# Performance work log

Hardware: AMD Instinct MI355X
Metric: run time of the kernel (lower is better)

The kernel has to match this reference:

```python
import jax, jax.numpy as jnp
import numpy as np

N = 100000
LS = (0, 1, 2)
MULS = (128, 64, 32)   # multiplicities of 0e,1o,2e in input1 / mid / out
MUL_Y = 64             # input2 = 64x0e (pure scalars)
DIM_X = sum(m * (2 * l + 1) for m, l in zip(MULS, LS))  # 480


def _split_irreps(x):
    # x: (N, 480) -> list of (N, mul, 2l+1) blocks
    parts, off = [], 0
    for m, l in zip(MULS, LS):
        d = m * (2 * l + 1)
        parts.append(x[:, off:off + d].reshape(-1, m, 2 * l + 1))
        off += d
    return parts


def setup_inputs() -> dict:
    key = jax.random.key(0)
    ks = jax.random.split(key, 8)
    inp = {
        "x": jax.random.normal(ks[0], (N, DIM_X), jnp.float32),
        "y": jax.random.normal(ks[1], (N, MUL_Y), jnp.float32),
    }
    for i, m in enumerate(MULS):
        # e3nn internal weights ~ N(0,1); path normalization applied in forward
        inp[f"W_tp{i}"] = jax.random.normal(ks[2 + i], (m, MUL_Y, m), jnp.float32)
        inp[f"W_lin{i}"] = jax.random.normal(ks[5 + i], (m, m), jnp.float32)
    return inp


def reference(x, y, W_tp0, W_tp1, W_tp2, W_lin0, W_lin1, W_lin2):
    W_tp = (W_tp0, W_tp1, W_tp2)
    W_lin = (W_lin0, W_lin1, W_lin2)
    xs = _split_irreps(x)
    outs = []
    for m, l, Wt, Wl, xl in zip(MULS, LS, W_tp, W_lin, xs):
        # e3nn 'uvw' path with scalar (0e) second input:
        #   CG(l,0,l)[m1,0,mo] = delta / sqrt(2l+1)
        #   path_weight = sqrt(ir_out.dim / (mul1*mul2)) = sqrt((2l+1)/(m*MUL_Y))
        # net coefficient = 1 / sqrt(m * MUL_Y)
        c_tp = float(1.0 / np.sqrt(m * MUL_Y))
        mid = c_tp * jnp.einsum('uvw,num,nv->nwm', Wt, xl, y)  # (N, m, 2l+1)
        # o3.Linear: single path per irrep, weight 1/sqrt(fan_in), fan_in = m
        c_lin = float(1.0 / np.sqrt(m))
        out = c_lin * jnp.einsum('uw,num->nwm', Wl, mid)       # (N, m, 2l+1)
        outs.append(out.reshape(-1, m * (2 * l + 1)))
    return jnp.concatenate(outs, axis=-1)  # (N, 480)
```

## Files before the change

kernel.cpp:

```cpp
#include <hip/hip_runtime.h>


typedef _Float16 f16x8 __attribute__((ext_vector_type(8)));
typedef _Float16 h2    __attribute__((ext_vector_type(2)));
typedef float    f32x4 __attribute__((ext_vector_type(4)));

template<int M, int NT>
__global__ void pack_b(const float* __restrict__ Wt, const float* __restrict__ Wl,
                       _Float16* __restrict__ Bp) {
    const int gid = blockIdx.x * 256 + threadIdx.x;
    const int total = M * 64 * M / 2;
    if (gid >= total) return;
    const int w_ = gid & (M - 1);
    const int uvp = gid / M;
    const float4* wtA = (const float4*)(Wt + (size_t)(2 * uvp) * M);
    const float4* wtB = (const float4*)(Wt + (size_t)(2 * uvp + 1) * M);
    float a0 = 0.f, a1 = 0.f;
    #pragma unroll 4
    for (int w = 0; w < M; w += 4) {
        float4 tA = wtA[w >> 2], tB = wtB[w >> 2];
        float l0 = Wl[(w + 0) * M + w_], l1 = Wl[(w + 1) * M + w_];
        float l2 = Wl[(w + 2) * M + w_], l3 = Wl[(w + 3) * M + w_];
        a0 += tA.x * l0 + tA.y * l1 + tA.z * l2 + tA.w * l3;
        a1 += tB.x * l0 + tB.y * l1 + tB.z * l2 + tB.w * l3;
    }
    #pragma unroll
    for (int t = 0; t < 2; ++t) {
        const int uv = 2 * uvp + t;
        const int u = uv >> 6, v = uv & 63;
        const int vh = v >> 5, vv = v & 31, quad = vv >> 3, j = vv & 7;
        const int kc = vh * M + u, nt = w_ >> 4, lane = quad * 16 + (w_ & 15);
        Bp[((size_t)(kc * NT + nt) * 64 + lane) * 8 + j] = (_Float16)(t ? a1 : a0);
    }
}

template<int M, int NCOMP, int XOFF, int NT, int MT, int WAVES_N, int LOGM>
__device__ __forceinline__ void tp_block(char* smem, int wg,
    const float* __restrict__ x, const float* __restrict__ y,
    const _Float16* __restrict__ Bp, float* __restrict__ out, int Rtot, float cscale)
{
    constexpr int YS = 80;
    constexpr int YROWS = (MT + NCOMP - 2) / NCOMP + 1;
    constexpr int KTOT = 2 * M;
    constexpr int SWZ = (2 * M >= 128) ? 8 : (2 * M) / 16;
    constexpr int WAVES_M = 4 / WAVES_N;
    constexpr int WM = (MT / 16) / WAVES_M;
    constexpr int WN = NT / WAVES_N;

    char* xb = smem;
    _Float16* yl = (_Float16*)(smem + MT * M * 2);
    const int tid = threadIdx.x;
    const int r0 = wg * MT;
    const int s0 = r0 / NCOMP;

    for (int idx = tid; idx < M * MT; idx += 256) {
        const int u = idx & (M - 1);
        const int row = idx >> LOGM;
        const int R = r0 + row;
        float v = 0.f;
        if (R < Rtot) {
            const int s = (unsigned)R / NCOMP;
            const int k = R - s * NCOMP;
            v = x[(size_t)s * 480 + XOFF + u * NCOMP + k];
        }
        const int off = ((row * M + u) * 2) ^ ((row & (SWZ - 1)) << 4);
        *(_Float16*)(xb + off) = (_Float16)v;
    }
    for (int idx = tid; idx < YROWS * 64; idx += 256) {
        const int v_ = idx & 63;
        const int row = idx >> 6;
        const int s = s0 + row;
        float val = 0.f;
        if (s * NCOMP < Rtot) val = y[(size_t)s * 64 + v_];
        yl[row * YS + v_] = (_Float16)val;
    }
    __syncthreads();

    const int lane = tid & 63;
    const int wv = tid >> 6;
    const int wni = wv % WAVES_N;
    const int wmi = wv / WAVES_N;
    const int l15 = lane & 15;
    const int quad = lane >> 4;

    int rowf[WM], xoffb[WM], yoffs[WM];
    #pragma unroll
    for (int f = 0; f < WM; ++f) {
        rowf[f] = (wmi * WM + f) * 16 + l15;
        xoffb[f] = (rowf[f] * M * 2) ^ ((rowf[f] & (SWZ - 1)) << 4);
        const int sloc = (int)((unsigned)(r0 + rowf[f]) / NCOMP) - s0;
        yoffs[f] = sloc * YS + quad * 8;
    }

    f32x4 acc[WM][WN];
    #pragma unroll
    for (int f = 0; f < WM; ++f)
        #pragma unroll
        for (int g = 0; g < WN; ++g) acc[f][g] = f32x4{0.f, 0.f, 0.f, 0.f};

    const char* bpc = (const char*)Bp;
    constexpr unsigned BSTRIDE = (unsigned)NT * 64 * 16;
    const unsigned lane_b = ((unsigned)(wni * WN) * 64 + lane) * 16;
    const unsigned bmax = (unsigned)(KTOT - 1) * BSTRIDE + lane_b;

    f16x8 bpp[2][WN];
    #pragma unroll
    for (int g = 0; g < WN; ++g) {
        bpp[0][g] = *(const f16x8*)(bpc + lane_b + g * 1024);
        bpp[1][g] = *(const f16x8*)(bpc + BSTRIDE + lane_b + g * 1024);
    }
    unsigned boff = 2 * BSTRIDE + lane_b;

    f16x8 xf[WM];
    uint4  yh[WM];

    #pragma unroll 1
    for (int g8 = 0; g8 < KTOT; g8 += 8) {
        const int u0 = g8 & (M - 1);
        #pragma unroll
        for (int f = 0; f < WM; ++f)
            xf[f] = *(const f16x8*)(xb + (xoffb[f] ^ (u0 * 2)));
        if (u0 == 0) {
            const int vh = g8 >> LOGM;
            #pragma unroll
            for (int f = 0; f < WM; ++f)
                yh[f] = *(const uint4*)(yl + yoffs[f] + vh * 32);
        }
        #pragma unroll
        for (int j = 0; j < 8; ++j) {
            f16x8 af[WM];
            #pragma unroll
            for (int f = 0; f < WM; ++f) {
                const _Float16 xh = xf[f][j];
                h2 xbb; xbb[0] = xh; xbb[1] = xh;
                union { uint4 u4; h2 h[4]; } yv; yv.u4 = yh[f];
                union { f16x8 v8; h2 h[4]; } a_;
                #pragma unroll
                for (int q = 0; q < 4; ++q) a_.h[q] = xbb * yv.h[q];
                af[f] = a_.v8;
            }
            #pragma unroll
            for (int f = 0; f < WM; ++f)
                #pragma unroll
                for (int g = 0; g < WN; ++g)
                    acc[f][g] = __builtin_amdgcn_mfma_f32_16x16x32_f16(af[f], bpp[j & 1][g], acc[f][g], 0, 0, 0);
            {
                const unsigned bo = boff < bmax ? boff : bmax;
                #pragma unroll
                for (int g = 0; g < WN; ++g)
                    bpp[j & 1][g] = *(const f16x8*)(bpc + bo + g * 1024);
                boff += BSTRIDE;
            }
        }
    }

    #pragma unroll
    for (int f = 0; f < WM; ++f) {
        #pragma unroll
        for (int g = 0; g < WN; ++g) {
            const int col = (wni * WN + g) * 16 + l15;
            #pragma unroll
            for (int r = 0; r < 4; ++r) {
                const int R = r0 + (wmi * WM + f) * 16 + quad * 4 + r;
                if (R < Rtot) {
                    const int s = (unsigned)R / NCOMP;
                    const int k = R - s * NCOMP;
                    out[(size_t)s * 480 + XOFF + col * NCOMP + k] = acc[f][g][r] * cscale;
                }
            }
        }
    }
}

__global__ __launch_bounds__(256, 3)
void tp_main(const float* __restrict__ x, const float* __restrict__ y,
             const _Float16* __restrict__ B0, const _Float16* __restrict__ B1,
             const _Float16* __restrict__ B2, float* __restrict__ out,
             int R0, int R1, int R2, int G0, int G1)
{
    __shared__ char smem[53248];
    const int b = blockIdx.x;
    if (b < G0)            tp_block<128, 1,   0, 8, 128, 2, 7>(smem, b,           x, y, B0, out, R0, 1.f / 1024.f);
    else if (b < G0 + G1)  tp_block< 64, 3, 128, 4, 128, 2, 6>(smem, b - G0,      x, y, B1, out, R1, 1.f / 512.f);
    else                   tp_block< 32, 5, 320, 2, 256, 1, 5>(smem, b - G0 - G1, x, y, B2, out, R2, 1.f / 256.f);
}

extern "C" void kernel_launch(void* const* d_in, const int* in_sizes, int n_in,
                              void* d_out, int out_size, void* d_ws, size_t ws_size,
                              hipStream_t stream) {
    const float* x   = (const float*)d_in[0];
    const float* y   = (const float*)d_in[1];
    const float* Wt0 = (const float*)d_in[2];
    const float* Wl0 = (const float*)d_in[3];
    const float* Wt1 = (const float*)d_in[4];
    const float* Wl1 = (const float*)d_in[5];
    const float* Wt2 = (const float*)d_in[6];
    const float* Wl2 = (const float*)d_in[7];
    float* out = (float*)d_out;

    const int Ns = in_sizes[0] / 480;

    _Float16* B0 = (_Float16*)d_ws;
    _Float16* B1 = B0 + 8192 * 128;
    _Float16* B2 = B1 + 4096 * 64;

    pack_b<128, 8><<<(128 * 64 * 128 / 2 + 255) / 256, 256, 0, stream>>>(Wt0, Wl0, B0);
    pack_b< 64, 4><<<( 64 * 64 *  64 / 2 + 255) / 256, 256, 0, stream>>>(Wt1, Wl1, B1);
    pack_b< 32, 2><<<( 32 * 64 *  32 / 2 + 255) / 256, 256, 0, stream>>>(Wt2, Wl2, B2);

    const int R0 = Ns, R1 = Ns * 3, R2 = Ns * 5;
    const int G0 = (R0 + 127) / 128;
    const int G1 = (R1 + 127) / 128;
    const int G2 = (R2 + 255) / 256;
    tp_main<<<G0 + G1 + G2, 256, 0, stream>>>(x, y, B0, B1, B2, out, R0, R1, R2, G0, G1);
}
```

Before: 818.5 us.

## Stage B tiles in LDS with async double buffering and larger row tiles

Reorders the packed B layout so K is interleaved by (u, v-half). The main loop now streams B chunks into LDS through global_load_lds with double buffering, instead of every wave loading B from global memory into registers. x is staged in 16-column slabs through a register prefetch and double-buffered LDS, and y is held directly in registers. Blocks grow to 512 threads and 384 or 512 rows, and each wave covers all N columns, so each B load is reused across more rows. The cost is one __syncthreads per K chunk, more registers per wave, and a larger LDS footprint per block, which limits how many blocks fit on a CU.

```diff
diff --git a/kernel.cpp b/kernel.cpp
--- a/kernel.cpp
+++ b/kernel.cpp
@@ -4,6 +4,12 @@
 typedef _Float16 f16x8 __attribute__((ext_vector_type(8)));
 typedef _Float16 h2    __attribute__((ext_vector_type(2)));
 typedef float    f32x4 __attribute__((ext_vector_type(4)));
+
+__device__ __forceinline__ void gload_lds16(const void* g, void* l) {
+    __builtin_amdgcn_global_load_lds(
+        (const __attribute__((address_space(1))) unsigned*)g,
+        (__attribute__((address_space(3))) unsigned*)l, 16, 0, 0);
+}
 
 template<int M, int NT>
 __global__ void pack_b(const float* __restrict__ Wt, const float* __restrict__ Wl,
@@ -29,141 +35,176 @@
         const int uv = 2 * uvp + t;
         const int u = uv >> 6, v = uv & 63;
         const int vh = v >> 5, vv = v & 31, quad = vv >> 3, j = vv & 7;
-        const int kc = vh * M + u, nt = w_ >> 4, lane = quad * 16 + (w_ & 15);
+        const int kc = u * 2 + vh, nt = w_ >> 4, lane = quad * 16 + (w_ & 15);
         Bp[((size_t)(kc * NT + nt) * 64 + lane) * 8 + j] = (_Float16)(t ? a1 : a0);
     }
 }
 
-template<int M, int NCOMP, int XOFF, int NT, int MT, int WAVES_N, int LOGM>
+template<int M, int NCOMP, int XOFF, int NT, int KC, int MT>
 __device__ __forceinline__ void tp_block(char* smem, int wg,
     const float* __restrict__ x, const float* __restrict__ y,
     const _Float16* __restrict__ Bp, float* __restrict__ out, int Rtot, float cscale)
 {
-    constexpr int YS = 80;
-    constexpr int YROWS = (MT + NCOMP - 2) / NCOMP + 1;
+    constexpr int WM = MT / 128;
+    constexpr int WN = NT;
+    constexpr int UC = KC / 2;
+    constexpr int XU = 16;
     constexpr int KTOT = 2 * M;
-    constexpr int SWZ = (2 * M >= 128) ? 8 : (2 * M) / 16;
-    constexpr int WAVES_M = 4 / WAVES_N;
-    constexpr int WM = (MT / 16) / WAVES_M;
-    constexpr int WN = NT / WAVES_N;
-
-    char* xb = smem;
-    _Float16* yl = (_Float16*)(smem + MT * M * 2);
+    constexpr int NCHUNK = KTOT / KC;
+    constexpr int CPS = XU / UC;
+    constexpr int NSLAB = M / XU;
+    constexpr int BCH = KC * NT * 1024;
+    constexpr int XSL = MT * XU * 2;
+    constexpr int NS_T = MT / NCOMP + 2;
+    constexpr int XE = NS_T * XU * NCOMP;
+    constexpr int XITER = (XE + 511) / 512;
+
+    char* bb0 = smem;
+    char* bb1 = smem + BCH;
+    char* xb0 = smem + 2 * BCH;
+    char* xb1 = smem + 2 * BCH + XSL;
+
     const int tid = threadIdx.x;
+    const int lane = tid & 63;
+    const int wv = tid >> 6;
+    const int l15 = lane & 15;
+    const int quad = lane >> 4;
     const int r0 = wg * MT;
     const int s0 = r0 / NCOMP;
-
-    for (int idx = tid; idx < M * MT; idx += 256) {
-        const int u = idx & (M - 1);
-        const int row = idx >> LOGM;
-        const int R = r0 + row;
-        float v = 0.f;
-        if (R < Rtot) {
-            const int s = (unsigned)R / NCOMP;
-            const int k = R - s * NCOMP;
-            v = x[(size_t)s * 480 + XOFF + u * NCOMP + k];
-        }
-        const int off = ((row * M + u) * 2) ^ ((row & (SWZ - 1)) << 4);
-        *(_Float16*)(xb + off) = (_Float16)v;
-    }
-    for (int idx = tid; idx < YROWS * 64; idx += 256) {
-        const int v_ = idx & 63;
-        const int row = idx >> 6;
-        const int s = s0 + row;
-        float val = 0.f;
-        if (s * NCOMP < Rtot) val = y[(size_t)s * 64 + v_];
-        yl[row * YS + v_] = (_Float16)val;
-    }
+    const int k0 = r0 - s0 * NCOMP;
+
+    float xt[XITER];
+    auto xld = [&](int slab) {
+        const int ub = slab * XU;
+        #pragma unroll
+        for (int i = 0; i < XITER; ++i) {
+            const int p = tid + i * 512;
+            float v = 0.f;
+            if (p < XE) {
+                const int sl = p / (XU * NCOMP);
+                const int fo = p - sl * (XU * NCOMP);
+                const int ul = fo / NCOMP;
+                const int k  = fo - ul * NCOMP;
+                const int rl = sl * NCOMP + k - k0;
+                if (rl >= 0 && rl < MT && (r0 + rl) < Rtot)
+                    v = x[(size_t)(s0 + sl) * 480 + XOFF + (ub + ul) * NCOMP + k];
+            }
+            xt[i] = v;
+        }
+    };
+    auto xwr = [&](char* xd) {
+        #pragma unroll
+        for (int i = 0; i < XITER; ++i) {
+            const int p = tid + i * 512;
+            if (p < XE) {
+                const int sl = p / (XU * NCOMP);
+                const int fo = p - sl * (XU * NCOMP);
+                const int ul = fo / NCOMP;
+                const int k  = fo - ul * NCOMP;
+                const int rl = sl * NCOMP + k - k0;
+                if (rl >= 0 && rl < MT)
+                    *(_Float16*)(xd + (rl * XU + ul) * 2) = (_Float16)xt[i];
+            }
+        }
+    };
+    auto stageB = [&](int c, char* bd) {
+        const char* gs = (const char*)Bp + (size_t)c * BCH + wv * 2048 + lane * 16;
+        char* ld = bd + wv * 2048;
+        gload_lds16(gs, ld);
+        gload_lds16(gs + 1024, ld + 1024);
+    };
+
+    int rowf[WM];
+    union YH { f16x8 v; h2 h[4]; };
+    YH yh[2][WM];
+    #pragma unroll
+    for (int f = 0; f < WM; ++f) {
+        rowf[f] = wv * (WM * 16) + f * 16 + l15;
+        const int Rg = r0 + rowf[f];
+        const int sf = (Rg < Rtot) ? (int)((unsigned)Rg / NCOMP) : 0;
+        #pragma unroll
+        for (int vh = 0; vh < 2; ++vh) {
+            const float4* yp = (const float4*)(y + (size_t)sf * 64 + vh * 32 + quad * 8);
+            const float4 a = yp[0], b = yp[1];
+            union { f16x8 v; _Float16 e[8]; } t;
+            t.e[0] = (_Float16)a.x; t.e[1] = (_Float16)a.y;
+            t.e[2] = (_Float16)a.z; t.e[3] = (_Float16)a.w;
+            t.e[4] = (_Float16)b.x; t.e[5] = (_Float16)b.y;
+            t.e[6] = (_Float16)b.z; t.e[7] = (_Float16)b.w;
+            yh[vh][f].v = t.v;
+        }
+    }
+
+    f32x4 acc[WM][WN];
+    #pragma unroll
+    for (int f = 0; f < WM; ++f)
+        #pragma unroll
+        for (int g = 0; g < WN; ++g) acc[f][g] = f32x4{0.f, 0.f, 0.f, 0.f};
+
+    xld(0);
+    stageB(0, bb0);
+    xwr(xb0);
     __syncthreads();
 
-    const int lane = tid & 63;
-    const int wv = tid >> 6;
-    const int wni = wv % WAVES_N;
-    const int wmi = wv / WAVES_N;
-    const int l15 = lane & 15;
-    const int quad = lane >> 4;
-
-    int rowf[WM], xoffb[WM], yoffs[WM];
-    #pragma unroll
-    for (int f = 0; f < WM; ++f) {
-        rowf[f] = (wmi * WM + f) * 16 + l15;
-        xoffb[f] = (rowf[f] * M * 2) ^ ((rowf[f] & (SWZ - 1)) << 4);
-        const int sloc = (int)((unsigned)(r0 + rowf[f]) / NCOMP) - s0;
-        yoffs[f] = sloc * YS + quad * 8;
-    }
-
-    f32x4 acc[WM][WN];
-    #pragma unroll
-    for (int f = 0; f < WM; ++f)
-        #pragma unroll
-        for (int g = 0; g < WN; ++g) acc[f][g] = f32x4{0.f, 0.f, 0.f, 0.f};
-
-    const char* bpc = (const char*)Bp;
-    constexpr unsigned BSTRIDE = (unsigned)NT * 64 * 16;
-    const unsigned lane_b = ((unsigned)(wni * WN) * 64 + lane) * 16;
-    const unsigned bmax = (unsigned)(KTOT - 1) * BSTRIDE + lane_b;
-
-    f16x8 bpp[2][WN];
-    #pragma unroll
-    for (int g = 0; g < WN; ++g) {
-        bpp[0][g] = *(const f16x8*)(bpc + lane_b + g * 1024);
-        bpp[1][g] = *(const f16x8*)(bpc + BSTRIDE + lane_b + g * 1024);
-    }
-    unsigned boff = 2 * BSTRIDE + lane_b;
-
-    f16x8 xf[WM];
-    uint4  yh[WM];
-
+    int bcur = 0, xcur = 0;
     #pragma unroll 1
-    for (int g8 = 0; g8 < KTOT; g8 += 8) {
-        const int u0 = g8 & (M - 1);
-        #pragma unroll
-        for (int f = 0; f < WM; ++f)
-            xf[f] = *(const f16x8*)(xb + (xoffb[f] ^ (u0 * 2)));
-        if (u0 == 0) {
-            const int vh = g8 >> LOGM;
-            #pragma unroll
-            for (int f = 0; f < WM; ++f)
-                yh[f] = *(const uint4*)(yl + yoffs[f] + vh * 32);
-        }
-        #pragma unroll
-        for (int j = 0; j < 8; ++j) {
+    for (int c = 0; c < NCHUNK; ++c) {
+        if (c + 1 < NCHUNK) stageB(c + 1, bcur ? bb0 : bb1);
+        const int cm = c & (CPS - 1);
+        const int sl1 = c / CPS + 1;
+        if (cm == 0 && sl1 < NSLAB) xld(sl1);
+
+        const char* bs = bcur ? bb1 : bb0;
+        const char* xs = xcur ? xb1 : xb0;
+        const int uoff = cm * UC;
+        unsigned xv0[WM], xv1[WM];
+        #pragma unroll
+        for (int f = 0; f < WM; ++f) {
+            const char* xa = xs + (rowf[f] * XU + uoff) * 2;
+            if constexpr (UC == 1)      xv0[f] = *(const unsigned short*)xa;
+            else if constexpr (UC == 2) xv0[f] = *(const unsigned*)xa;
+            else { const uint2 t = *(const uint2*)xa; xv0[f] = t.x; xv1[f] = t.y; }
+        }
+        #pragma unroll
+        for (int kl = 0; kl < KC; ++kl) {
+            const int vh = kl & 1, uo = kl >> 1;
+            f16x8 bg[WN];
+            #pragma unroll
+            for (int g = 0; g < WN; ++g)
+                bg[g] = *(const f16x8*)(bs + (kl * NT + g) * 1024 + lane * 16);
             f16x8 af[WM];
             #pragma unroll
             for (int f = 0; f < WM; ++f) {
-                const _Float16 xh = xf[f][j];
-                h2 xbb; xbb[0] = xh; xbb[1] = xh;
-                union { uint4 u4; h2 h[4]; } yv; yv.u4 = yh[f];
-                union { f16x8 v8; h2 h[4]; } a_;
+                const unsigned d = (UC == 4 && (uo & 2)) ? xv1[f] : xv0[f];
+                const unsigned hh = (uo & 1) ? (d >> 16) : (d & 0xffffu);
+                union { unsigned u; h2 h; } xb2; xb2.u = hh | (hh << 16);
+                union { f16x8 v; h2 h[4]; } a_;
                 #pragma unroll
-                for (int q = 0; q < 4; ++q) a_.h[q] = xbb * yv.h[q];
-                af[f] = a_.v8;
+                for (int q = 0; q < 4; ++q) a_.h[q] = xb2.h * yh[vh][f].h[q];
+                af[f] = a_.v;
             }
             #pragma unroll
             for (int f = 0; f < WM; ++f)
                 #pragma unroll
                 for (int g = 0; g < WN; ++g)
-                    acc[f][g] = __builtin_amdgcn_mfma_f32_16x16x32_f16(af[f], bpp[j & 1][g], acc[f][g], 0, 0, 0);
-            {
-                const unsigned bo = boff < bmax ? boff : bmax;
-                #pragma unroll
-                for (int g = 0; g < WN; ++g)
-                    bpp[j & 1][g] = *(const f16x8*)(bpc + bo + g * 1024);
-                boff += BSTRIDE;
-            }
-        }
+                    acc[f][g] = __builtin_amdgcn_mfma_f32_16x16x32_f16(af[f], bg[g], acc[f][g], 0, 0, 0);
+        }
+        if (cm == CPS - 1 && sl1 < NSLAB) xwr(xcur ? xb0 : xb1);
+        __syncthreads();
+        bcur ^= 1;
+        if (cm == CPS - 1) xcur ^= 1;
     }
 
     #pragma unroll
     for (int f = 0; f < WM; ++f) {
         #pragma unroll
         for (int g = 0; g < WN; ++g) {
-            const int col = (wni * WN + g) * 16 + l15;
+            const int col = g * 16 + l15;
             #pragma unroll
             for (int r = 0; r < 4; ++r) {
-                const int R = r0 + (wmi * WM + f) * 16 + quad * 4 + r;
+                const int R = r0 + wv * (WM * 16) + f * 16 + quad * 4 + r;
                 if (R < Rtot) {
-                    const int s = (unsigned)R / NCOMP;
+                    const int s = (int)((unsigned)R / NCOMP);
                     const int k = R - s * NCOMP;
                     out[(size_t)s * 480 + XOFF + col * NCOMP + k] = acc[f][g][r] * cscale;
                 }
@@ -172,17 +213,17 @@
     }
 }
 
-__global__ __launch_bounds__(256, 3)
+__global__ __launch_bounds__(512, 2)
 void tp_main(const float* __restrict__ x, const float* __restrict__ y,
              const _Float16* __restrict__ B0, const _Float16* __restrict__ B1,
              const _Float16* __restrict__ B2, float* __restrict__ out,
              int R0, int R1, int R2, int G0, int G1)
 {
-    __shared__ char smem[53248];
+    __shared__ char smem[65536];
     const int b = blockIdx.x;
-    if (b < G0)            tp_block<128, 1,   0, 8, 128, 2, 7>(smem, b,           x, y, B0, out, R0, 1.f / 1024.f);
-    else if (b < G0 + G1)  tp_block< 64, 3, 128, 4, 128, 2, 6>(smem, b - G0,      x, y, B1, out, R1, 1.f / 512.f);
-    else                   tp_block< 32, 5, 320, 2, 256, 1, 5>(smem, b - G0 - G1, x, y, B2, out, R2, 1.f / 256.f);
+    if (b < G0)            tp_block<128, 1,   0, 8, 2, 384>(smem, b,           x, y, B0, out, R0, 1.f / 1024.f);
+    else if (b < G0 + G1)  tp_block< 64, 3, 128, 4, 4, 512>(smem, b - G0,      x, y, B1, out, R1, 1.f / 512.f);
+    else                   tp_block< 32, 5, 320, 2, 8, 512>(smem, b - G0 - G1, x, y, B2, out, R2, 1.f / 256.f);
 }
 
 extern "C" void kernel_launch(void* const* d_in, const int* in_sizes, int n_in,
@@ -209,8 +250,8 @@
     pack_b< 32, 2><<<( 32 * 64 *  32 / 2 + 255) / 256, 256, 0, stream>>>(Wt2, Wl2, B2);
 
     const int R0 = Ns, R1 = Ns * 3, R2 = Ns * 5;
-    const int G0 = (R0 + 127) / 128;
-    const int G1 = (R1 + 127) / 128;
-    const int G2 = (R2 + 255) / 256;
-    tp_main<<<G0 + G1 + G2, 256, 0, stream>>>(x, y, B0, B1, B2, out, R0, R1, R2, G0, G1);
-}
+    const int G0 = (R0 + 383) / 384;
+    const int G1 = (R1 + 511) / 512;
+    const int G2 = (R2 + 511) / 512;
+    tp_main<<<G0 + G1 + G2, 512, 0, stream>>>(x, y, B0, B1, B2, out, R0, R1, R2, G0, G1);
+}
```

After: 682.1 us. -16.7%, faster.
